# Kernel optimization log

Hardware: AMD Instinct MI355X
Metric: run time of the kernel (lower is better)

## Reference

```python
import jax, jax.numpy as jnp
import numpy as np

F_FD = 16      # fdfilter
XLEN = 128     # grid side
BS, CH = 16, 4


def _conv(x, w):
    # x: [N, Cin, H, W], w: [Cout, Cin, kh, kw], VALID, stride 1
    return jax.lax.conv_general_dilated(
        x, w, window_strides=(1, 1), padding='VALID',
        dimension_numbers=('NCHW', 'OIHW', 'NCHW'))


def setup_inputs() -> dict:
    key = jax.random.key(0)
    ks = jax.random.split(key, 14)
    s = 0.1
    F = F_FD
    inp = {
        'xInput': jax.random.normal(ks[0], (BS, CH, XLEN, XLEN), dtype=jnp.float32),
        'wX1':  jax.random.normal(ks[1],  (F, 1, 1, 3), dtype=jnp.float32) * s,
        'wX1L': jax.random.normal(ks[2],  (F, 1, 1, 2), dtype=jnp.float32) * s,
        'wX1R': jax.random.normal(ks[3],  (F, 1, 1, 2), dtype=jnp.float32) * s,
        'wY1':  jax.random.normal(ks[4],  (F, 1, 3, 1), dtype=jnp.float32) * s,
        'wY1L': jax.random.normal(ks[5],  (F, 1, 2, 1), dtype=jnp.float32) * s,
        'wY1R': jax.random.normal(ks[6],  (F, 1, 2, 1), dtype=jnp.float32) * s,
        'wX2':  jax.random.normal(ks[7],  (F, F, 1, 3), dtype=jnp.float32) * s,
        'wX2L': jax.random.normal(ks[8],  (F, F, 1, 2), dtype=jnp.float32) * s,
        'wX2R': jax.random.normal(ks[9],  (F, F, 1, 2), dtype=jnp.float32) * s,
        'wY2':  jax.random.normal(ks[10], (F, F, 3, 1), dtype=jnp.float32) * s,
        'wY2L': jax.random.normal(ks[11], (F, F, 2, 1), dtype=jnp.float32) * s,
        'wY2R': jax.random.normal(ks[12], (F, F, 2, 1), dtype=jnp.float32) * s,
        'wfc':  jax.random.normal(ks[13], (1, 4 * F), dtype=jnp.float32) * s,
        'fdblock': 8,
    }
    return inp


def reference(xInput, wX1, wX1L, wX1R, wY1, wY1L, wY1R,
              wX2, wX2L, wX2R, wY2, wY2L, wY2R, wfc, fdblock):
    BS_, C_, H, W = xInput.shape
    x = xInput.reshape(-1, 1, H, W)  # fold channels into batch, Cin=1
    for _ in range(fdblock):
        # first-order x/y finite-difference stencils with boundary convs
        dX = jnp.concatenate([_conv(x[:, :, :, :2], wX1L),
                              _conv(x, wX1),
                              _conv(x[:, :, :, -2:], wX1R)], axis=3)
        dY = jnp.concatenate([_conv(x[:, :, :2, :], wY1L),
                              _conv(x, wY1),
                              _conv(x[:, :, -2:, :], wY1R)], axis=2)
        # second-order stencils on the first-order fields
        dX2 = jnp.concatenate([_conv(dX[:, :, :, :2], wX2L),
                               _conv(dX, wX2),
                               _conv(dX[:, :, :, -2:], wX2R)], axis=3)
        dY2 = jnp.concatenate([_conv(dY[:, :, :2, :], wY2L),
                               _conv(dY, wY2),
                               _conv(dY[:, :, -2:, :], wY2R)], axis=2)
        combine = jnp.concatenate([dX, dY, dX2, dY2], axis=1)  # [N, 4F, H, W]
        # fc over channel dim (transpose(1,3)+Linear+transpose(1,3) == channel contraction)
        deviation = jnp.einsum('nchw,oc->nohw', combine, wfc)  # [N, 1, H, W]
        x = x + deviation
    return x.reshape(BS_, C_, H, W)
```

## Files before the change

kernel.cpp:

```cpp
#include <hip/hip_runtime.h>

#define F 16
#define XL 128


__device__ __forceinline__ float g1f(const float* __restrict__ w1,
                                     const float* __restrict__ w1L,
                                     const float* __restrict__ w1R,
                                     int f, int v, int wp) {
  if (v == 0) {
    if (wp == 0) return w1L[f * 2 + 0];
    if (wp == 1) return w1L[f * 2 + 1];
    return 0.f;
  }
  if (v == XL - 1) {
    if (wp == XL - 2) return w1R[f * 2 + 0];
    if (wp == XL - 1) return w1R[f * 2 + 1];
    return 0.f;
  }
  int k = wp - (v - 1);
  return (k >= 0 && k < 3) ? w1[f * 3 + k] : 0.f;
}

__global__ __launch_bounds__(512)
void fd_fused_kernel(const float* __restrict__ x_in,
                     const float* __restrict__ wX1, const float* __restrict__ wX1L,
                     const float* __restrict__ wX1R, const float* __restrict__ wY1,
                     const float* __restrict__ wY1L, const float* __restrict__ wY1R,
                     const float* __restrict__ wX2, const float* __restrict__ wX2L,
                     const float* __restrict__ wX2R, const float* __restrict__ wY2,
                     const float* __restrict__ wY2L, const float* __restrict__ wY2R,
                     const float* __restrict__ wfc, const int* __restrict__ fdp,
                     float* __restrict__ x_out) {
  __shared__ __align__(16) float buf[2][64 * XL];
  __shared__ __align__(16) float rbl[5][XL];
  __shared__ __align__(16) float cbl[5][XL];
  __shared__ float r1s[2][3], r1Ls[2][2], r1Rs[2][2];
  __shared__ float qs[2][F][3], qLs[2][F][2], qRs[2][F][2];

  const int tid = threadIdx.x;
  const int n = blockIdx.x >> 2;
  const int s = blockIdx.x & 3;
  const int g0 = (s == 0) ? 0 : (s == 1) ? 16 : (s == 2) ? 48 : 64;
  const int l0 = (s == 0) ? 0 : (s == 3) ? 32 : 16;

  {
    const float4* sg4 = (const float4*)(x_in + n * (XL * XL) + g0 * XL);
    float4* b4 = (float4*)buf[0];
#pragma unroll
    for (int i = 0; i < 4; ++i) b4[tid + 512 * i] = sg4[tid + 512 * i];
  }

  {
    const int t = tid;
    if (t < 6) {
      int p = t / 3, k = t % 3;
      const float* w1 = p ? wY1 : wX1;
      int off = p ? F : 0;
      float sm = 0.f;
      for (int f = 0; f < F; ++f) sm += wfc[off + f] * w1[f * 3 + k];
      r1s[p][k] = sm;
    } else if (t < 10) {
      int t2 = t - 6; int p = t2 / 2, k = t2 % 2;
      const float* w1L = p ? wY1L : wX1L;
      int off = p ? F : 0;
      float sm = 0.f;
      for (int f = 0; f < F; ++f) sm += wfc[off + f] * w1L[f * 2 + k];
      r1Ls[p][k] = sm;
    } else if (t < 14) {
      int t2 = t - 10; int p = t2 / 2, k = t2 % 2;
      const float* w1R = p ? wY1R : wX1R;
      int off = p ? F : 0;
      float sm = 0.f;
      for (int f = 0; f < F; ++f) sm += wfc[off + f] * w1R[f * 2 + k];
      r1Rs[p][k] = sm;
    } else if (t < 14 + 96) {
      int t2 = t - 14; int p = t2 / 48; int r = t2 % 48; int fi = r / 3, k = r % 3;
      const float* w2 = p ? wY2 : wX2;
      int off = p ? 3 * F : 2 * F;
      float sm = 0.f;
      for (int fo = 0; fo < F; ++fo) sm += wfc[off + fo] * w2[(fo * F + fi) * 3 + k];
      qs[p][fi][k] = sm;
    } else if (t < 110 + 64) {
      int t2 = t - 110; int p = t2 / 32; int r = t2 % 32; int fi = r / 2, k = r % 2;
      const float* w2L = p ? wY2L : wX2L;
      int off = p ? 3 * F : 2 * F;
      float sm = 0.f;
      for (int fo = 0; fo < F; ++fo) sm += wfc[off + fo] * w2L[(fo * F + fi) * 2 + k];
      qLs[p][fi][k] = sm;
    } else if (t < 174 + 64) {
      int t2 = t - 174; int p = t2 / 32; int r = t2 % 32; int fi = r / 2, k = r % 2;
      const float* w2R = p ? wY2R : wX2R;
      int off = p ? 3 * F : 2 * F;
      float sm = 0.f;
      for (int fo = 0; fo < F; ++fo) sm += wfc[off + fo] * w2R[(fo * F + fi) * 2 + k];
      qRs[p][fi][k] = sm;
    }
  }
  __syncthreads();

  for (int e = tid; e < 2 * 5 * XL; e += 512) {
    const int pp = e / (5 * XL);
    const int rem = e % (5 * XL);
    const int w = rem / 5;
    const int d = rem % 5;
    const int wp = w + d - 2;
    const float* w1  = pp ? wY1  : wX1;
    const float* w1L = pp ? wY1L : wX1L;
    const float* w1R = pp ? wY1R : wX1R;
    float c = 0.f;
    if (wp >= 0 && wp < XL) {
      if (w == 0) {
        if (wp == 0)       c += r1Ls[pp][0];
        else if (wp == 1)  c += r1Ls[pp][1];
      } else if (w == XL - 1) {
        if (wp == XL - 2)      c += r1Rs[pp][0];
        else if (wp == XL - 1) c += r1Rs[pp][1];
      } else {
        int k = wp - (w - 1);
        if (k >= 0 && k < 3) c += r1s[pp][k];
      }
      if (w == 0) {
        for (int vi = 0; vi < 2; ++vi)
          for (int fi = 0; fi < F; ++fi)
            c += qLs[pp][fi][vi] * g1f(w1, w1L, w1R, fi, vi, wp);
      } else if (w == XL - 1) {
        for (int vi = 0; vi < 2; ++vi)
          for (int fi = 0; fi < F; ++fi)
            c += qRs[pp][fi][vi] * g1f(w1, w1L, w1R, fi, XL - 2 + vi, wp);
      } else {
        for (int k2 = 0; k2 < 3; ++k2) {
          int v = w - 1 + k2;
          for (int fi = 0; fi < F; ++fi)
            c += qs[pp][fi][k2] * g1f(w1, w1L, w1R, fi, v, wp);
        }
      }
    }
    if (pp == 0) rbl[d][w] = c; else cbl[d][w] = c;
  }
  __syncthreads();

  const int q = tid & 31;
  const int rbase = (tid >> 5) << 2;
  const int plm = (q > 0) ? 2 * q - 1 : 0;
  const int prm = (q < 31) ? 2 * q + 2 : 63;

  const float4 rb0 = ((const float4*)rbl[0])[q];
  const float4 rb1 = ((const float4*)rbl[1])[q];
  const float4 rb2 = ((const float4*)rbl[2])[q];
  const float4 rb3 = ((const float4*)rbl[3])[q];
  const float4 rb4 = ((const float4*)rbl[4])[q];
  const float cbi0 = cbl[0][64];
  const float cbi1 = cbl[1][64];
  const float cbi2 = cbl[2][64];
  const float cbi3 = cbl[3][64];
  const float cbi4 = cbl[4][64];

  const int fdb = fdp[0];
  float4* out4 = (float4*)(x_out + n * (XL * XL));

  if (fdb == 0) {
    const float4* bc = (const float4*)buf[0];
#pragma unroll
    for (int j = 0; j < 4; ++j) {
      const int r = rbase + j;
      const int lr = r - l0;
      if (lr >= 0 && lr < 32) out4[(32 * s + lr) * 32 + q] = bc[r * 32 + q];
    }
    return;
  }

  for (int t = 0; t < fdb; ++t) {
    const float4* bc  = (const float4*)buf[t & 1];
    const float2* bc2 = (const float2*)buf[t & 1];
    float4* bn = (float4*)buf[(t & 1) ^ 1];
    const bool last = (t == fdb - 1);

    float4 c_m2 = bc[((rbase >= 2) ? rbase - 2 : 0) * 32 + q];
    float4 c_m1 = bc[((rbase >= 1) ? rbase - 1 : 0) * 32 + q];
    float4 c_0  = bc[(rbase + 0) * 32 + q];
    float4 c_p1 = bc[(rbase + 1) * 32 + q];
    float4 c_p2 = bc[(rbase + 2) * 32 + q];

#pragma unroll
    for (int j = 0; j < 4; ++j) {
      const int r = rbase + j;
      const int gh = g0 + r;
      const float2 hl = bc2[r * 64 + plm];
      const float2 hr = bc2[r * 64 + prm];
      float b0 = cbi0, b1 = cbi1, b2 = cbi2, b3 = cbi3, b4c = cbi4;
      if (gh < 2 || gh > 125) {
        b0 = cbl[0][gh]; b1 = cbl[1][gh]; b2 = cbl[2][gh];
        b3 = cbl[3][gh]; b4c = cbl[4][gh];
      }
      float4 a;
      a.x = c_0.x
        + rb0.x * hl.x  + rb1.x * hl.y  + rb2.x * c_0.x + rb3.x * c_0.y + rb4.x * c_0.z
        + b0 * c_m2.x + b1 * c_m1.x + b2 * c_0.x + b3 * c_p1.x + b4c * c_p2.x;
      a.y = c_0.y
        + rb0.y * hl.y  + rb1.y * c_0.x + rb2.y * c_0.y + rb3.y * c_0.z + rb4.y * c_0.w
        + b0 * c_m2.y + b1 * c_m1.y + b2 * c_0.y + b3 * c_p1.y + b4c * c_p2.y;
      a.z = c_0.z
        + rb0.z * c_0.x + rb1.z * c_0.y + rb2.z * c_0.z + rb3.z * c_0.w + rb4.z * hr.x
        + b0 * c_m2.z + b1 * c_m1.z + b2 * c_0.z + b3 * c_p1.z + b4c * c_p2.z;
      a.w = c_0.w
        + rb0.w * c_0.y + rb1.w * c_0.z + rb2.w * c_0.w + rb3.w * hr.x  + rb4.w * hr.y
        + b0 * c_m2.w + b1 * c_m1.w + b2 * c_0.w + b3 * c_p1.w + b4c * c_p2.w;

      if (!last) {
        bn[r * 32 + q] = a;
      } else {
        const int lr = r - l0;
        if (lr >= 0 && lr < 32) out4[(32 * s + lr) * 32 + q] = a;
      }
      c_m2 = c_m1; c_m1 = c_0; c_0 = c_p1; c_p1 = c_p2;
      const int rn = (r + 3 <= 63) ? r + 3 : 63;
      c_p2 = bc[rn * 32 + q];
    }
    if (!last) __syncthreads();
  }
}

extern "C" void kernel_launch(void* const* d_in, const int* in_sizes, int n_in,
                              void* d_out, int out_size, void* d_ws, size_t ws_size,
                              hipStream_t stream) {
  const float* xInput = (const float*)d_in[0];
  const float* wX1  = (const float*)d_in[1];
  const float* wX1L = (const float*)d_in[2];
  const float* wX1R = (const float*)d_in[3];
  const float* wY1  = (const float*)d_in[4];
  const float* wY1L = (const float*)d_in[5];
  const float* wY1R = (const float*)d_in[6];
  const float* wX2  = (const float*)d_in[7];
  const float* wX2L = (const float*)d_in[8];
  const float* wX2R = (const float*)d_in[9];
  const float* wY2  = (const float*)d_in[10];
  const float* wY2L = (const float*)d_in[11];
  const float* wY2R = (const float*)d_in[12];
  const float* wfc  = (const float*)d_in[13];
  const int*   fdp  = (const int*)d_in[14];

  float* out = (float*)d_out;

  fd_fused_kernel<<<256, 512, 0, stream>>>(xInput, wX1, wX1L, wX1R, wY1, wY1L, wY1R,
                                           wX2, wX2L, wX2R, wY2, wY2L, wY2R,
                                           wfc, fdp, out);
}
```

Before: 108.7 us.

## Keep stencil tile in registers with DPP row shifts and two-step halo exchange

Reworks the fused finite-difference kernel so each thread holds a 2-row by 8-column patch in registers. Vertical neighbours come from adjacent lanes via DPP row shifts, and horizontal halos are exchanged through a small shared buffer. A 4-column halo lets two timesteps run per synchronisation, replacing the full 64x128 shared double buffer and a barrier per step. The costs are redundant halo compute and more register pressure. The DPP shift is row-limited (16 lanes), which risks wrong values at row boundaries unless the lane mapping accounts for it.

Result: slower. 111.6 us (+2.7%).

```diff
diff --git a/kernel.cpp b/kernel.cpp
--- a/kernel.cpp
+++ b/kernel.cpp
@@ -3,6 +3,14 @@
 #define F 16
 #define XL 128
 
+__device__ __forceinline__ float dpp_shr1(float x) {
+  return __int_as_float(
+      __builtin_amdgcn_update_dpp(0, __float_as_int(x), 0x138, 0xf, 0xf, true));
+}
+__device__ __forceinline__ float dpp_shl1(float x) {
+  return __int_as_float(
+      __builtin_amdgcn_update_dpp(0, __float_as_int(x), 0x130, 0xf, 0xf, true));
+}
 
 __device__ __forceinline__ float g1f(const float* __restrict__ w1,
                                      const float* __restrict__ w1L,
@@ -22,33 +30,72 @@
   return (k >= 0 && k < 3) ? w1[f * 3 + k] : 0.f;
 }
 
-__global__ __launch_bounds__(512)
-void fd_fused_kernel(const float* __restrict__ x_in,
-                     const float* __restrict__ wX1, const float* __restrict__ wX1L,
-                     const float* __restrict__ wX1R, const float* __restrict__ wY1,
-                     const float* __restrict__ wY1L, const float* __restrict__ wY1R,
-                     const float* __restrict__ wX2, const float* __restrict__ wX2L,
-                     const float* __restrict__ wX2R, const float* __restrict__ wY2,
-                     const float* __restrict__ wY2L, const float* __restrict__ wY2R,
-                     const float* __restrict__ wfc, const int* __restrict__ fdp,
-                     float* __restrict__ x_out) {
-  __shared__ __align__(16) float buf[2][64 * XL];
-  __shared__ __align__(16) float rbl[5][XL];
-  __shared__ __align__(16) float cbl[5][XL];
+struct Cf {
+  float rbi[5], rbe0[5], rbe1[5], rbe6[5], rbe7[5], cb0[5], cb1[5];
+};
+
+template <int OUTN, int KLO>
+__device__ __forceinline__ void stepT(const float (&e0)[OUTN + 4], const float (&e1)[OUTN + 4],
+                                      float (&o0)[OUTN], float (&o1)[OUTN], const Cf& cf) {
+#pragma unroll
+  for (int j = 0; j < OUTN; ++j) {
+    const int k = KLO + j;
+    float c0b, c1b, c2b, c3b, c4b;
+    if (k == 0)      { c0b = cf.rbe0[0]; c1b = cf.rbe0[1]; c2b = cf.rbe0[2]; c3b = cf.rbe0[3]; c4b = cf.rbe0[4]; }
+    else if (k == 1) { c0b = cf.rbe1[0]; c1b = cf.rbe1[1]; c2b = cf.rbe1[2]; c3b = cf.rbe1[3]; c4b = cf.rbe1[4]; }
+    else if (k == 6) { c0b = cf.rbe6[0]; c1b = cf.rbe6[1]; c2b = cf.rbe6[2]; c3b = cf.rbe6[3]; c4b = cf.rbe6[4]; }
+    else if (k == 7) { c0b = cf.rbe7[0]; c1b = cf.rbe7[1]; c2b = cf.rbe7[2]; c3b = cf.rbe7[3]; c4b = cf.rbe7[4]; }
+    else             { c0b = cf.rbi[0];  c1b = cf.rbi[1];  c2b = cf.rbi[2];  c3b = cf.rbi[3];  c4b = cf.rbi[4];  }
+    const float a0 = e0[j + 2], a1 = e1[j + 2];
+    const float vm2 = dpp_shr1(a0);
+    const float vm1 = dpp_shr1(a1);
+    const float vp2 = dpp_shl1(a0);
+    const float vp3 = dpp_shl1(a1);
+    o0[j] = a0
+      + c0b * e0[j] + c1b * e0[j + 1] + c2b * a0 + c3b * e0[j + 3] + c4b * e0[j + 4]
+      + cf.cb0[0] * vm2 + cf.cb0[1] * vm1 + cf.cb0[2] * a0 + cf.cb0[3] * a1 + cf.cb0[4] * vp2;
+    o1[j] = a1
+      + c0b * e1[j] + c1b * e1[j + 1] + c2b * a1 + c3b * e1[j + 3] + c4b * e1[j + 4]
+      + cf.cb1[0] * vm1 + cf.cb1[1] * a0 + cf.cb1[2] * a1 + cf.cb1[3] * vp2 + cf.cb1[4] * vp3;
+  }
+}
+
+__global__ __launch_bounds__(512, 2)
+void fd_fused2_kernel(const float* __restrict__ x_in,
+                      const float* __restrict__ wX1, const float* __restrict__ wX1L,
+                      const float* __restrict__ wX1R, const float* __restrict__ wY1,
+                      const float* __restrict__ wY1L, const float* __restrict__ wY1R,
+                      const float* __restrict__ wX2, const float* __restrict__ wX2L,
+                      const float* __restrict__ wX2R, const float* __restrict__ wY2,
+                      const float* __restrict__ wY2L, const float* __restrict__ wY2R,
+                      const float* __restrict__ wfc, const int* __restrict__ fdp,
+                      float* __restrict__ x_out) {
+  __shared__ float4 hb[2][8][2][2][64];
+  __shared__ float rbl[5][XL], cbl[5][XL];
   __shared__ float r1s[2][3], r1Ls[2][2], r1Rs[2][2];
   __shared__ float qs[2][F][3], qLs[2][F][2], qRs[2][F][2];
 
   const int tid = threadIdx.x;
+  const int z = tid & 63;
+  const int w = tid >> 6;
   const int n = blockIdx.x >> 2;
   const int s = blockIdx.x & 3;
-  const int g0 = (s == 0) ? 0 : (s == 1) ? 16 : (s == 2) ? 48 : 64;
-  const int l0 = (s == 0) ? 0 : (s == 3) ? 32 : 16;
-
+  int cs0 = 32 * s - 16; if (cs0 < 0) cs0 = 0; if (cs0 > 64) cs0 = 64;
+  const int c0 = cs0 + 8 * w;
+  const int r0 = 2 * z, r1 = 2 * z + 1;
+
+  float f0[8], f1[8];
   {
-    const float4* sg4 = (const float4*)(x_in + n * (XL * XL) + g0 * XL);
-    float4* b4 = (float4*)buf[0];
-#pragma unroll
-    for (int i = 0; i < 4; ++i) b4[tid + 512 * i] = sg4[tid + 512 * i];
+    const float* img = x_in + n * XL * XL;
+    const float4* a = (const float4*)(img + r0 * XL + c0);
+    const float4* b = (const float4*)(img + r1 * XL + c0);
+#pragma unroll
+    for (int m = 0; m < 2; ++m) {
+      const float4 v = a[m];
+      f0[4 * m] = v.x; f0[4 * m + 1] = v.y; f0[4 * m + 2] = v.z; f0[4 * m + 3] = v.w;
+      const float4 u = b[m];
+      f1[4 * m] = u.x; f1[4 * m + 1] = u.y; f1[4 * m + 2] = u.z; f1[4 * m + 3] = u.w;
+    }
   }
 
   {
@@ -102,122 +149,121 @@
   for (int e = tid; e < 2 * 5 * XL; e += 512) {
     const int pp = e / (5 * XL);
     const int rem = e % (5 * XL);
-    const int w = rem / 5;
+    const int ww = rem / 5;
     const int d = rem % 5;
-    const int wp = w + d - 2;
+    const int wp = ww + d - 2;
     const float* w1  = pp ? wY1  : wX1;
     const float* w1L = pp ? wY1L : wX1L;
     const float* w1R = pp ? wY1R : wX1R;
     float c = 0.f;
     if (wp >= 0 && wp < XL) {
-      if (w == 0) {
+      if (ww == 0) {
         if (wp == 0)       c += r1Ls[pp][0];
         else if (wp == 1)  c += r1Ls[pp][1];
-      } else if (w == XL - 1) {
+      } else if (ww == XL - 1) {
         if (wp == XL - 2)      c += r1Rs[pp][0];
         else if (wp == XL - 1) c += r1Rs[pp][1];
       } else {
-        int k = wp - (w - 1);
+        int k = wp - (ww - 1);
         if (k >= 0 && k < 3) c += r1s[pp][k];
       }
-      if (w == 0) {
+      if (ww == 0) {
         for (int vi = 0; vi < 2; ++vi)
           for (int fi = 0; fi < F; ++fi)
             c += qLs[pp][fi][vi] * g1f(w1, w1L, w1R, fi, vi, wp);
-      } else if (w == XL - 1) {
+      } else if (ww == XL - 1) {
         for (int vi = 0; vi < 2; ++vi)
           for (int fi = 0; fi < F; ++fi)
             c += qRs[pp][fi][vi] * g1f(w1, w1L, w1R, fi, XL - 2 + vi, wp);
       } else {
         for (int k2 = 0; k2 < 3; ++k2) {
-          int v = w - 1 + k2;
+          int v = ww - 1 + k2;
           for (int fi = 0; fi < F; ++fi)
             c += qs[pp][fi][k2] * g1f(w1, w1L, w1R, fi, v, wp);
         }
       }
     }
-    if (pp == 0) rbl[d][w] = c; else cbl[d][w] = c;
+    if (pp == 0) rbl[d][ww] = c; else cbl[d][ww] = c;
   }
   __syncthreads();
 
-  const int q = tid & 31;
-  const int rbase = (tid >> 5) << 2;
-  const int plm = (q > 0) ? 2 * q - 1 : 0;
-  const int prm = (q < 31) ? 2 * q + 2 : 63;
-
-  const float4 rb0 = ((const float4*)rbl[0])[q];
-  const float4 rb1 = ((const float4*)rbl[1])[q];
-  const float4 rb2 = ((const float4*)rbl[2])[q];
-  const float4 rb3 = ((const float4*)rbl[3])[q];
-  const float4 rb4 = ((const float4*)rbl[4])[q];
-  const float cbi0 = cbl[0][64];
-  const float cbi1 = cbl[1][64];
-  const float cbi2 = cbl[2][64];
-  const float cbi3 = cbl[3][64];
-  const float cbi4 = cbl[4][64];
+  Cf cf;
+#pragma unroll
+  for (int d = 0; d < 5; ++d) {
+    cf.rbi[d]  = rbl[d][64];
+    cf.rbe0[d] = rbl[d][c0];
+    cf.rbe1[d] = rbl[d][c0 + 1];
+    cf.rbe6[d] = rbl[d][c0 + 6];
+    cf.rbe7[d] = rbl[d][c0 + 7];
+    cf.cb0[d]  = cbl[d][r0];
+    cf.cb1[d]  = cbl[d][r1];
+  }
 
   const int fdb = fdp[0];
-  float4* out4 = (float4*)(x_out + n * (XL * XL));
-
-  if (fdb == 0) {
-    const float4* bc = (const float4*)buf[0];
-#pragma unroll
-    for (int j = 0; j < 4; ++j) {
-      const int r = rbase + j;
-      const int lr = r - l0;
-      if (lr >= 0 && lr < 32) out4[(32 * s + lr) * 32 + q] = bc[r * 32 + q];
-    }
-    return;
-  }
-
-  for (int t = 0; t < fdb; ++t) {
-    const float4* bc  = (const float4*)buf[t & 1];
-    const float2* bc2 = (const float2*)buf[t & 1];
-    float4* bn = (float4*)buf[(t & 1) ^ 1];
-    const bool last = (t == fdb - 1);
-
-    float4 c_m2 = bc[((rbase >= 2) ? rbase - 2 : 0) * 32 + q];
-    float4 c_m1 = bc[((rbase >= 1) ? rbase - 1 : 0) * 32 + q];
-    float4 c_0  = bc[(rbase + 0) * 32 + q];
-    float4 c_p1 = bc[(rbase + 1) * 32 + q];
-    float4 c_p2 = bc[(rbase + 2) * 32 + q];
-
-#pragma unroll
-    for (int j = 0; j < 4; ++j) {
-      const int r = rbase + j;
-      const int gh = g0 + r;
-      const float2 hl = bc2[r * 64 + plm];
-      const float2 hr = bc2[r * 64 + prm];
-      float b0 = cbi0, b1 = cbi1, b2 = cbi2, b3 = cbi3, b4c = cbi4;
-      if (gh < 2 || gh > 125) {
-        b0 = cbl[0][gh]; b1 = cbl[1][gh]; b2 = cbl[2][gh];
-        b3 = cbl[3][gh]; b4c = cbl[4][gh];
-      }
-      float4 a;
-      a.x = c_0.x
-        + rb0.x * hl.x  + rb1.x * hl.y  + rb2.x * c_0.x + rb3.x * c_0.y + rb4.x * c_0.z
-        + b0 * c_m2.x + b1 * c_m1.x + b2 * c_0.x + b3 * c_p1.x + b4c * c_p2.x;
-      a.y = c_0.y
-        + rb0.y * hl.y  + rb1.y * c_0.x + rb2.y * c_0.y + rb3.y * c_0.z + rb4.y * c_0.w
-        + b0 * c_m2.y + b1 * c_m1.y + b2 * c_0.y + b3 * c_p1.y + b4c * c_p2.y;
-      a.z = c_0.z
-        + rb0.z * c_0.x + rb1.z * c_0.y + rb2.z * c_0.z + rb3.z * c_0.w + rb4.z * hr.x
-        + b0 * c_m2.z + b1 * c_m1.z + b2 * c_0.z + b3 * c_p1.z + b4c * c_p2.z;
-      a.w = c_0.w
-        + rb0.w * c_0.y + rb1.w * c_0.z + rb2.w * c_0.w + rb3.w * hr.x  + rb4.w * hr.y
-        + b0 * c_m2.w + b1 * c_m1.w + b2 * c_0.w + b3 * c_p1.w + b4c * c_p2.w;
-
-      if (!last) {
-        bn[r * 32 + q] = a;
-      } else {
-        const int lr = r - l0;
-        if (lr >= 0 && lr < 32) out4[(32 * s + lr) * 32 + q] = a;
-      }
-      c_m2 = c_m1; c_m1 = c_0; c_0 = c_p1; c_p1 = c_p2;
-      const int rn = (r + 3 <= 63) ? r + 3 : 63;
-      c_p2 = bc[rn * 32 + q];
-    }
-    if (!last) __syncthreads();
+  const int nd = fdb >> 1;
+  const int odd = fdb & 1;
+  const int wl = (w > 0) ? w - 1 : 0;
+  const int wr = (w < 7) ? w + 1 : 7;
+
+  for (int t = 0; t < nd; ++t) {
+    const int b = t & 1;
+    hb[b][w][0][0][z] = make_float4(f0[0], f0[1], f0[2], f0[3]);
+    hb[b][w][0][1][z] = make_float4(f1[0], f1[1], f1[2], f1[3]);
+    hb[b][w][1][0][z] = make_float4(f0[4], f0[5], f0[6], f0[7]);
+    hb[b][w][1][1][z] = make_float4(f1[4], f1[5], f1[6], f1[7]);
+    __syncthreads();
+    const float4 lA = hb[b][wl][1][0][z];
+    const float4 lB = hb[b][wl][1][1][z];
+    const float4 rA = hb[b][wr][0][0][z];
+    const float4 rB = hb[b][wr][0][1][z];
+
+    float e0[16], e1[16];
+    e0[0] = lA.x; e0[1] = lA.y; e0[2] = lA.z; e0[3] = lA.w;
+    e1[0] = lB.x; e1[1] = lB.y; e1[2] = lB.z; e1[3] = lB.w;
+#pragma unroll
+    for (int k = 0; k < 8; ++k) { e0[4 + k] = f0[k]; e1[4 + k] = f1[k]; }
+    e0[12] = rA.x; e0[13] = rA.y; e0[14] = rA.z; e0[15] = rA.w;
+    e1[12] = rB.x; e1[13] = rB.y; e1[14] = rB.z; e1[15] = rB.w;
+
+    float t0[12], t1[12];
+    stepT<12, -2>(e0, e1, t0, t1, cf);
+    stepT<8, 0>(t0, t1, f0, f1, cf);
+  }
+
+  if (odd) {
+    const int b = nd & 1;
+    hb[b][w][0][0][z] = make_float4(f0[0], f0[1], f0[2], f0[3]);
+    hb[b][w][0][1][z] = make_float4(f1[0], f1[1], f1[2], f1[3]);
+    hb[b][w][1][0][z] = make_float4(f0[4], f0[5], f0[6], f0[7]);
+    hb[b][w][1][1][z] = make_float4(f1[4], f1[5], f1[6], f1[7]);
+    __syncthreads();
+    const float4 lA = hb[b][wl][1][0][z];
+    const float4 lB = hb[b][wl][1][1][z];
+    const float4 rA = hb[b][wr][0][0][z];
+    const float4 rB = hb[b][wr][0][1][z];
+    float e0[12], e1[12];
+    e0[0] = lA.z; e0[1] = lA.w;
+    e1[0] = lB.z; e1[1] = lB.w;
+#pragma unroll
+    for (int k = 0; k < 8; ++k) { e0[2 + k] = f0[k]; e1[2 + k] = f1[k]; }
+    e0[10] = rA.x; e0[11] = rA.y;
+    e1[10] = rB.x; e1[11] = rB.y;
+    float o0[8], o1[8];
+    stepT<8, 0>(e0, e1, o0, o1, cf);
+#pragma unroll
+    for (int k = 0; k < 8; ++k) { f0[k] = o0[k]; f1[k] = o1[k]; }
+  }
+
+  const int rel = c0 - 32 * s;
+  if (rel >= 0 && rel < 32) {
+    float* outp = x_out + n * XL * XL;
+    float4* o0p = (float4*)(outp + r0 * XL + c0);
+    float4* o1p = (float4*)(outp + r1 * XL + c0);
+#pragma unroll
+    for (int m = 0; m < 2; ++m) {
+      o0p[m] = make_float4(f0[4 * m], f0[4 * m + 1], f0[4 * m + 2], f0[4 * m + 3]);
+      o1p[m] = make_float4(f1[4 * m], f1[4 * m + 1], f1[4 * m + 2], f1[4 * m + 3]);
+    }
   }
 }
 
@@ -242,7 +288,7 @@
 
   float* out = (float*)d_out;
 
-  fd_fused_kernel<<<256, 512, 0, stream>>>(xInput, wX1, wX1L, wX1R, wY1, wY1L, wY1R,
-                                           wX2, wX2L, wX2R, wY2, wY2L, wY2R,
-                                           wfc, fdp, out);
-}
+  fd_fused2_kernel<<<256, 512, 0, stream>>>(xInput, wX1, wX1L, wX1R, wY1, wY1L, wY1R,
+                                            wX2, wX2L, wX2R, wY2, wY2L, wY2R,
+                                            wfc, fdp, out);
+}
```
